# Kernel tuning notes

Measured on AMD Instinct MI355X. Metric: run time of the kernel, lower is better.

## Reference

```python
import jax, jax.numpy as jnp
import numpy as np

WS = 12
NUM_HEADS = 6
EPS = 1e-5


def _ln(x, w, b):
    mu = jnp.mean(x, axis=-1, keepdims=True)
    var = jnp.var(x, axis=-1, keepdims=True)
    return (x - mu) * jax.lax.rsqrt(var + EPS) * w + b


def _lin(x, w, b):
    return jnp.einsum('...i,oi->...o', x, w) + b


def _window_partition(x, ws):
    # x: [B, C, H, W] -> [B*Nh*Nw, ws*ws, C]
    B, C, H, W = x.shape
    x = x.reshape(B, C, H // ws, ws, W // ws, ws)
    x = jnp.transpose(x, (0, 2, 4, 3, 5, 1))
    return x.reshape(-1, ws * ws, C)


def _window_reverse(win, ws, B, C, H, W):
    Nh, Nw = H // ws, W // ws
    x = win.reshape(B, Nh, Nw, ws, ws, C)
    x = jnp.transpose(x, (0, 5, 1, 3, 2, 4))
    return x.reshape(B, C, H, W)


def setup_inputs() -> dict:
    key = jax.random.key(0)
    ks = jax.random.split(key, 12)
    B, C, H, W = 4, 192, 240, 240
    hid = 4 * C
    s = 0.02
    return {
        'opt': jax.random.normal(ks[0], (B, C, H, W), jnp.float32),
        'sar': jax.random.normal(ks[1], (B, C, H, W), jnp.float32),
        'ln_q_w': jnp.ones((C,), jnp.float32), 'ln_q_b': jnp.zeros((C,), jnp.float32),
        'ln_kv_w': jnp.ones((C,), jnp.float32), 'ln_kv_b': jnp.zeros((C,), jnp.float32),
        'wq': jax.random.normal(ks[2], (C, C), jnp.float32) * s, 'bq': jnp.zeros((C,), jnp.float32),
        'wk': jax.random.normal(ks[3], (C, C), jnp.float32) * s, 'bk': jnp.zeros((C,), jnp.float32),
        'wv': jax.random.normal(ks[4], (C, C), jnp.float32) * s, 'bv': jnp.zeros((C,), jnp.float32),
        'wp': jax.random.normal(ks[5], (C, C), jnp.float32) * s, 'bp': jnp.zeros((C,), jnp.float32),
        'gw1': jax.random.normal(ks[6], (C, C), jnp.float32) * s, 'gb1': jnp.zeros((C,), jnp.float32),
        'gw2': jax.random.normal(ks[7], (C, C), jnp.float32) * s, 'gb2': jnp.zeros((C,), jnp.float32),
        'gamma': jnp.float32(0.1),
        'ln_o_w': jnp.ones((C,), jnp.float32), 'ln_o_b': jnp.zeros((C,), jnp.float32),
        'w1': jax.random.normal(ks[8], (hid, C), jnp.float32) * s, 'b1': jnp.zeros((hid,), jnp.float32),
        'w2': jax.random.normal(ks[9], (C, hid), jnp.float32) * s, 'b2': jnp.zeros((C,), jnp.float32),
    }


def reference(opt, sar, ln_q_w, ln_q_b, ln_kv_w, ln_kv_b, wq, bq, wk, bk, wv, bv,
              wp, bp, gw1, gb1, gw2, gb2, gamma, ln_o_w, ln_o_b, w1, b1, w2, b2):
    B, C, H, W = opt.shape
    Hh = NUM_HEADS
    hd = C // Hh
    scale = hd ** -0.5

    opt_tok = _window_partition(opt, WS)   # [Bn, N, C]
    sar_tok = _window_partition(sar, WS)
    Bn, N, _ = opt_tok.shape

    opt_ln = _ln(opt_tok, ln_q_w, ln_q_b)
    sar_ln = _ln(sar_tok, ln_kv_w, ln_kv_b)

    q = _lin(opt_ln, wq, bq).reshape(Bn, N, Hh, hd)
    k = _lin(sar_ln, wk, bk).reshape(Bn, N, Hh, hd)
    v = _lin(sar_ln, wv, bv).reshape(Bn, N, Hh, hd)

    attn = jnp.einsum('bnhd,bmhd->bhnm', q, k) * scale
    attn = jax.nn.softmax(attn, axis=-1)
    out = jnp.einsum('bhnm,bmhd->bnhd', attn, v).reshape(Bn, N, C)
    fused = _lin(out, wp, bp)

    # sigmoid gate on mean-pooled sar tokens
    g = jax.nn.sigmoid(_lin(jax.nn.gelu(_lin(jnp.mean(sar_ln, axis=1), gw1, gb1), approximate=False), gw2, gb2))
    fused = opt_tok + gamma * (g[:, None, :] * fused)

    h = _ln(fused, ln_o_w, ln_o_b)
    h = _lin(jax.nn.gelu(_lin(h, w1, b1), approximate=False), w2, b2)
    fused = fused + h

    return _window_reverse(fused, WS, B, C, H, W)
```

## Files before the change

### kernel.cpp

```cpp
#include <hip/hip_runtime.h>
#include <hip/hip_bf16.h>

#define ROWS 230400
#define CDIM 192
#define NTOK 144
#define NWIN 1600
#define PLANE 57600
#define HDIM 768

typedef __attribute__((ext_vector_type(8))) short bf16x8;
typedef __attribute__((ext_vector_type(4))) float f32x4;

__device__ __forceinline__ ushort f2bf(float f) {
  union { float f; unsigned u; } v; v.f = f;
  unsigned r = v.u + 0x7FFFu + ((v.u >> 16) & 1u);
  return (ushort)(r >> 16);
}
__device__ __forceinline__ float bf2f(ushort h) {
  union { unsigned u; float f; } v; v.u = ((unsigned)h) << 16;
  return v.f;
}
__device__ __forceinline__ float gelu_f(float x) {
  return 0.5f * x * (1.f + erff(x * 0.7071067811865475f));
}

struct CvtJobs {
  const float* src[8];
  ushort* dst[8];
  int n[8];
};
__global__ __launch_bounds__(256) void cvt_kernel(CvtJobs jobs) {
  int stride = gridDim.x * blockDim.x;
  int t0 = blockIdx.x * blockDim.x + threadIdx.x;
  for (int j = 0; j < 8; ++j) {
    const float* s = jobs.src[j]; ushort* d = jobs.dst[j]; int n = jobs.n[j];
    for (int e = t0; e < n; e += stride) d[e] = f2bf(s[e]);
  }
}

__global__ __launch_bounds__(256) void lnpart_kernel(
    const float* __restrict__ opt, const float* __restrict__ sar,
    const float* __restrict__ lnqw, const float* __restrict__ lnqb,
    const float* __restrict__ lnkw, const float* __restrict__ lnkb,
    ushort* __restrict__ opt_ln, ushort* __restrict__ sar_ln,
    ushort* __restrict__ opt_tok) {
  __shared__ __align__(16) ushort X[NTOK * 200];
  __shared__ float smu[NTOK], srs[NTOK];
  int win = blockIdx.x;
  int b = win / 400, rr = win % 400, nh = rr / 20, nw = rr % 20;
  size_t wbase = (size_t)b * CDIM * PLANE + (size_t)(nh * 12) * 240 + nw * 12;
  int tid = threadIdx.x;
  for (int pass = 0; pass < 2; ++pass) {
    const float* src = pass ? sar : opt;
    for (int e = tid; e < CDIM * 36; e += 256) {
      int c = e / 36, r2 = e % 36, i = r2 / 3, j0 = (r2 % 3) * 4;
      float4 v = *(const float4*)&src[wbase + (size_t)c * PLANE + i * 240 + j0];
      int tok = i * 12 + j0;
      X[(tok + 0) * 200 + c] = f2bf(v.x);
      X[(tok + 1) * 200 + c] = f2bf(v.y);
      X[(tok + 2) * 200 + c] = f2bf(v.z);
      X[(tok + 3) * 200 + c] = f2bf(v.w);
    }
    __syncthreads();
    if (tid < NTOK) {
      float s = 0.f, qs = 0.f;
      for (int c = 0; c < CDIM; ++c) { float v = bf2f(X[tid * 200 + c]); s += v; qs += v * v; }
      float mu = s * (1.f / CDIM);
      smu[tid] = mu;
      srs[tid] = rsqrtf(qs * (1.f / CDIM) - mu * mu + 1e-5f);
    }
    __syncthreads();
    const float* w = pass ? lnkw : lnqw;
    const float* bb = pass ? lnkb : lnqb;
    ushort* dst = pass ? sar_ln : opt_ln;
    for (int e = tid; e < NTOK * CDIM; e += 256) {
      int tok = e / CDIM, c = e % CDIM;
      ushort raw = X[tok * 200 + c];
      float v = bf2f(raw);
      float y = (v - smu[tok]) * srs[tok] * w[c] + bb[c];
      size_t o = (size_t)(win * NTOK + tok) * CDIM + c;
      dst[o] = f2bf(y);
      if (!pass) opt_tok[o] = raw;
    }
    __syncthreads();
  }
}

enum { EPI_BF16 = 0, EPI_GELU = 1, EPI_SIG = 2, EPI_PROJ = 3 };

template <int EPI>
__global__ __launch_bounds__(256) void gemm_kernel(
    const ushort* __restrict__ A, const ushort* __restrict__ Wt,
    const float* __restrict__ bias, const float* __restrict__ bias2,
    void* __restrict__ outp, int M, int N, int K,
    const float* __restrict__ g, const ushort* __restrict__ opt_tok,
    const float* __restrict__ gamma_p) {
  __shared__ __align__(16) ushort Alds[128 * 40];
  int m0 = blockIdx.x * 128;
  int n0 = blockIdx.y * 64;
  int tid = threadIdx.x;
  int wave = tid >> 6, lane = tid & 63, ls = lane & 15, quad = lane >> 4;
  f32x4 acc[2][4] = {};
  for (int k0 = 0; k0 < K; k0 += 32) {
    for (int it = 0; it < 2; ++it) {
      int ch = tid + 256 * it;
      int r = ch >> 2, c8 = (ch & 3) * 8;
      int grow = m0 + r; if (grow > M - 1) grow = M - 1;
      *(bf16x8*)&Alds[r * 40 + c8] = *(const bf16x8*)&A[(size_t)grow * K + k0 + c8];
    }
    __syncthreads();
    int mb = wave * 32;
    bf16x8 af0 = *(const bf16x8*)&Alds[(mb + ls) * 40 + quad * 8];
    bf16x8 af1 = *(const bf16x8*)&Alds[(mb + 16 + ls) * 40 + quad * 8];
    bf16x8 bfr[4];
    for (int nf = 0; nf < 4; ++nf)
      bfr[nf] = *(const bf16x8*)&Wt[(size_t)(n0 + nf * 16 + ls) * K + k0 + quad * 8];
    for (int nf = 0; nf < 4; ++nf) {
      acc[0][nf] = __builtin_amdgcn_mfma_f32_16x16x32_bf16(af0, bfr[nf], acc[0][nf], 0, 0, 0);
      acc[1][nf] = __builtin_amdgcn_mfma_f32_16x16x32_bf16(af1, bfr[nf], acc[1][nf], 0, 0, 0);
    }
    __syncthreads();
  }
  float gam = (EPI == EPI_PROJ) ? gamma_p[0] : 0.f;
  for (int s = 0; s < 2; ++s) {
    int rowbase = m0 + wave * 32 + s * 16 + quad * 4;
    for (int nf = 0; nf < 4; ++nf) {
      int col = n0 + nf * 16 + ls;
      float bb = (col < 192) ? bias[col] : bias2[col - 192];
      for (int r = 0; r < 4; ++r) {
        int row = rowbase + r;
        if (row >= M) continue;
        float v = acc[s][nf][r] + bb;
        if (EPI == EPI_BF16) {
          ((ushort*)outp)[(size_t)row * N + col] = f2bf(v);
        } else if (EPI == EPI_GELU) {
          ((ushort*)outp)[(size_t)row * N + col] = f2bf(gelu_f(v));
        } else if (EPI == EPI_SIG) {
          ((float*)outp)[(size_t)row * N + col] = 1.f / (1.f + __expf(-v));
        } else {
          int win = row / NTOK;
          float gv = g[(size_t)win * CDIM + col];
          float ov = bf2f(opt_tok[(size_t)row * CDIM + col]);
          ((ushort*)outp)[(size_t)row * CDIM + col] = f2bf(ov + gam * gv * v);
        }
      }
    }
  }
}

__global__ __launch_bounds__(192) void pool_kernel(const ushort* __restrict__ sar_ln,
                                                   ushort* __restrict__ pool) {
  int win = blockIdx.x, c = threadIdx.x;
  float s = 0.f;
  size_t base = (size_t)win * NTOK * CDIM + c;
  for (int t = 0; t < NTOK; ++t) s += bf2f(sar_ln[base + (size_t)t * CDIM]);
  pool[(size_t)win * CDIM + c] = f2bf(s * (1.f / NTOK));
}

__global__ __launch_bounds__(256) void attn_kernel(const ushort* __restrict__ q,
                                                   const ushort* __restrict__ kv,
                                                   ushort* __restrict__ attn_out) {
  __shared__ __align__(16) ushort vT[32 * 168];
  __shared__ __align__(16) ushort P[4][16 * 168];
  int blk = blockIdx.x;
  int win = blk / 6, head = blk % 6;
  int tid = threadIdx.x, wave = tid >> 6, lane = tid & 63, ls = lane & 15, quad = lane >> 4;
  size_t qbase = (size_t)win * NTOK * CDIM + head * 32;
  size_t kbase = (size_t)win * NTOK * 384 + head * 32;
  size_t vbase = kbase + 192;
  for (int e = tid; e < NTOK * 32; e += 256) {
    int t = e >> 5, d = e & 31;
    vT[d * 168 + t] = kv[vbase + (size_t)t * 384 + d];
  }
  for (int e = tid; e < 32 * 24; e += 256) {
    int d = e / 24, j = 144 + e % 24;
    vT[d * 168 + j] = 0;
  }
  __syncthreads();
  const float scale = 0.17677669529663687f;
  ushort* Pw = P[wave];
  f32x4 zero = {0.f, 0.f, 0.f, 0.f};
  for (int mt = wave; mt < 9; mt += 4) {
    int m0 = mt * 16;
    bf16x8 aq = *(const bf16x8*)&q[qbase + (size_t)(m0 + ls) * CDIM + quad * 8];
    f32x4 S[9];
    for (int nt = 0; nt < 9; ++nt) {
      bf16x8 bk = *(const bf16x8*)&kv[kbase + (size_t)(nt * 16 + ls) * 384 + quad * 8];
      S[nt] = __builtin_amdgcn_mfma_f32_16x16x32_bf16(aq, bk, zero, 0, 0, 0);
    }
    for (int nt = 0; nt < 9; ++nt)
      for (int r = 0; r < 4; ++r) S[nt][r] *= scale;
    for (int r = 0; r < 4; ++r) {
      float mx = -1e30f;
      for (int nt = 0; nt < 9; ++nt) mx = fmaxf(mx, S[nt][r]);
      for (int o = 1; o < 16; o <<= 1) mx = fmaxf(mx, __shfl_xor(mx, o));
      float sm = 0.f;
      for (int nt = 0; nt < 9; ++nt) { float e = __expf(S[nt][r] - mx); S[nt][r] = e; sm += e; }
      for (int o = 1; o < 16; o <<= 1) sm += __shfl_xor(sm, o);
      float inv = 1.f / sm;
      for (int nt = 0; nt < 9; ++nt)
        Pw[(quad * 4 + r) * 168 + nt * 16 + ls] = f2bf(S[nt][r] * inv);
    }
    for (int e = lane; e < 16 * 24; e += 64) {
      int r = e / 24, j = 144 + e % 24;
      Pw[r * 168 + j] = 0;
    }
    f32x4 O[2] = {};
    for (int ks = 0; ks < 5; ++ks) {
      bf16x8 ap = *(const bf16x8*)&Pw[ls * 168 + ks * 32 + quad * 8];
      for (int dt = 0; dt < 2; ++dt) {
        bf16x8 bv = *(const bf16x8*)&vT[(dt * 16 + ls) * 168 + ks * 32 + quad * 8];
        O[dt] = __builtin_amdgcn_mfma_f32_16x16x32_bf16(ap, bv, O[dt], 0, 0, 0);
      }
    }
    for (int dt = 0; dt < 2; ++dt)
      for (int r = 0; r < 4; ++r)
        attn_out[(size_t)(win * NTOK + m0 + quad * 4 + r) * CDIM + head * 32 + dt * 16 + ls] =
            f2bf(O[dt][r]);
  }
}

__global__ __launch_bounds__(256) void lno_kernel(const ushort* __restrict__ x,
                                                  const float* __restrict__ w,
                                                  const float* __restrict__ b,
                                                  ushort* __restrict__ out) {
  int row = blockIdx.x * 4 + (threadIdx.x >> 6);
  int lane = threadIdx.x & 63;
  const ushort* xr = x + (size_t)row * CDIM;
  float v[3], s = 0.f, qs = 0.f;
  for (int i = 0; i < 3; ++i) { v[i] = bf2f(xr[lane + 64 * i]); s += v[i]; qs += v[i] * v[i]; }
  for (int o = 1; o < 64; o <<= 1) { s += __shfl_xor(s, o); qs += __shfl_xor(qs, o); }
  float mu = s * (1.f / CDIM);
  float rs = rsqrtf(qs * (1.f / CDIM) - mu * mu + 1e-5f);
  ushort* orow = out + (size_t)row * CDIM;
  for (int i = 0; i < 3; ++i) {
    int c = lane + 64 * i;
    orow[c] = f2bf((v[i] - mu) * rs * w[c] + b[c]);
  }
}

__global__ __launch_bounds__(256, 2) void mlp_kernel(
    const ushort* __restrict__ h, const ushort* __restrict__ fused,
    const ushort* __restrict__ w1b, const float* __restrict__ b1,
    const ushort* __restrict__ w2b, const float* __restrict__ b2,
    ushort* __restrict__ y) {
  __shared__ __align__(16) ushort Hs[128 * 200];
  __shared__ __align__(16) ushort Ts[128 * 72];
  int m0 = blockIdx.x * 128;
  int tid = threadIdx.x, wave = tid >> 6, lane = tid & 63, ls = lane & 15, quad = lane >> 4;
  for (int it = 0; it < 12; ++it) {
    int ch = tid + 256 * it;
    int r = ch / 24, c8 = (ch % 24) * 8;
    *(bf16x8*)&Hs[r * 200 + c8] = *(const bf16x8*)&h[(size_t)(m0 + r) * CDIM + c8];
  }
  __syncthreads();
  int mb = wave * 32;
  f32x4 acc[2][12] = {};
  for (int hc = 0; hc < HDIM; hc += 64) {
    f32x4 t[2][4] = {};
    for (int ks = 0; ks < 6; ++ks) {
      bf16x8 a0 = *(const bf16x8*)&Hs[(mb + ls) * 200 + ks * 32 + quad * 8];
      bf16x8 a1 = *(const bf16x8*)&Hs[(mb + 16 + ls) * 200 + ks * 32 + quad * 8];
      for (int nf = 0; nf < 4; ++nf) {
        bf16x8 bw = *(const bf16x8*)&w1b[(size_t)(hc + nf * 16 + ls) * CDIM + ks * 32 + quad * 8];
        t[0][nf] = __builtin_amdgcn_mfma_f32_16x16x32_bf16(a0, bw, t[0][nf], 0, 0, 0);
        t[1][nf] = __builtin_amdgcn_mfma_f32_16x16x32_bf16(a1, bw, t[1][nf], 0, 0, 0);
      }
    }
    for (int s = 0; s < 2; ++s)
      for (int nf = 0; nf < 4; ++nf) {
        float bb = b1[hc + nf * 16 + ls];
        for (int r = 0; r < 4; ++r) {
          float v = gelu_f(t[s][nf][r] + bb);
          Ts[(mb + s * 16 + quad * 4 + r) * 72 + nf * 16 + ls] = f2bf(v);
        }
      }
    for (int ks = 0; ks < 2; ++ks) {
      bf16x8 a0 = *(const bf16x8*)&Ts[(mb + ls) * 72 + ks * 32 + quad * 8];
      bf16x8 a1 = *(const bf16x8*)&Ts[(mb + 16 + ls) * 72 + ks * 32 + quad * 8];
      for (int nf = 0; nf < 12; ++nf) {
        bf16x8 bw = *(const bf16x8*)&w2b[(size_t)(nf * 16 + ls) * HDIM + hc + ks * 32 + quad * 8];
        acc[0][nf] = __builtin_amdgcn_mfma_f32_16x16x32_bf16(a0, bw, acc[0][nf], 0, 0, 0);
        acc[1][nf] = __builtin_amdgcn_mfma_f32_16x16x32_bf16(a1, bw, acc[1][nf], 0, 0, 0);
      }
    }
  }
  for (int s = 0; s < 2; ++s)
    for (int nf = 0; nf < 12; ++nf) {
      float bb = b2[nf * 16 + ls];
      for (int r = 0; r < 4; ++r) {
        size_t idx = (size_t)(m0 + mb + s * 16 + quad * 4 + r) * CDIM + nf * 16 + ls;
        y[idx] = f2bf(bf2f(fused[idx]) + acc[s][nf][r] + bb);
      }
    }
}

__global__ __launch_bounds__(256) void unpart_kernel(const ushort* __restrict__ y,
                                                     float* __restrict__ out) {
  __shared__ __align__(16) ushort X[NTOK * 200];
  int win = blockIdx.x;
  int b = win / 400, rr = win % 400, nh = rr / 20, nw = rr % 20;
  size_t wbase = (size_t)b * CDIM * PLANE + (size_t)(nh * 12) * 240 + nw * 12;
  int tid = threadIdx.x;
  for (int e = tid; e < NTOK * 24; e += 256) {
    int tok = e / 24, c8 = (e % 24) * 8;
    *(bf16x8*)&X[tok * 200 + c8] = *(const bf16x8*)&y[(size_t)(win * NTOK + tok) * CDIM + c8];
  }
  __syncthreads();
  for (int e = tid; e < CDIM * 36; e += 256) {
    int c = e / 36, r2 = e % 36, i = r2 / 3, j0 = (r2 % 3) * 4;
    int tok = i * 12 + j0;
    float4 v;
    v.x = bf2f(X[(tok + 0) * 200 + c]);
    v.y = bf2f(X[(tok + 1) * 200 + c]);
    v.z = bf2f(X[(tok + 2) * 200 + c]);
    v.w = bf2f(X[(tok + 3) * 200 + c]);
    *(float4*)&out[wbase + (size_t)c * PLANE + i * 240 + j0] = v;
  }
}

extern "C" void kernel_launch(void* const* d_in, const int* in_sizes, int n_in,
                              void* d_out, int out_size, void* d_ws, size_t ws_size,
                              hipStream_t stream) {
  const float* opt   = (const float*)d_in[0];
  const float* sar   = (const float*)d_in[1];
  const float* lnqw  = (const float*)d_in[2];
  const float* lnqb  = (const float*)d_in[3];
  const float* lnkw  = (const float*)d_in[4];
  const float* lnkb  = (const float*)d_in[5];
  const float* wq    = (const float*)d_in[6];
  const float* bq    = (const float*)d_in[7];
  const float* wk    = (const float*)d_in[8];
  const float* bk    = (const float*)d_in[9];
  const float* wv    = (const float*)d_in[10];
  const float* bv    = (const float*)d_in[11];
  const float* wp    = (const float*)d_in[12];
  const float* bp    = (const float*)d_in[13];
  const float* gw1   = (const float*)d_in[14];
  const float* gb1   = (const float*)d_in[15];
  const float* gw2   = (const float*)d_in[16];
  const float* gb2   = (const float*)d_in[17];
  const float* gamma = (const float*)d_in[18];
  const float* lnow  = (const float*)d_in[19];
  const float* lnob  = (const float*)d_in[20];
  const float* w1    = (const float*)d_in[21];
  const float* b1    = (const float*)d_in[22];
  const float* w2    = (const float*)d_in[23];
  const float* b2    = (const float*)d_in[24];

  char* ws = (char*)d_ws;
  size_t off = 0;
  auto take = [&](size_t bytes) -> char* {
    char* p = ws + off;
    off += (bytes + 255) & ~(size_t)255;
    return p;
  };
  const size_t big = (size_t)ROWS * CDIM * 2;
  ushort* opt_ln  = (ushort*)take(big);
  ushort* sar_ln  = (ushort*)take(big);
  ushort* opt_tok = (ushort*)take(big);
  ushort* qb      = (ushort*)take(big);
  ushort* kv      = (ushort*)take((size_t)ROWS * 384 * 2);
  ushort* wq_bf   = (ushort*)take(CDIM * CDIM * 2);
  ushort* wkv_bf  = (ushort*)take(2 * CDIM * CDIM * 2);
  ushort* wp_bf   = (ushort*)take(CDIM * CDIM * 2);
  ushort* w1_bf   = (ushort*)take((size_t)HDIM * CDIM * 2);
  ushort* w2_bf   = (ushort*)take((size_t)CDIM * HDIM * 2);
  ushort* gw1_bf  = (ushort*)take(CDIM * CDIM * 2);
  ushort* gw2_bf  = (ushort*)take(CDIM * CDIM * 2);
  ushort* pool_bf = (ushort*)take(NWIN * CDIM * 2);
  ushort* g1_bf   = (ushort*)take(NWIN * CDIM * 2);
  float*  g_f     = (float*)take(NWIN * CDIM * 4);
  ushort* h        = opt_ln;
  ushort* attn_out = sar_ln;
  ushort* fused    = qb;
  ushort* yb       = sar_ln;

  CvtJobs jobs;
  jobs.src[0] = wq;  jobs.dst[0] = wq_bf;               jobs.n[0] = CDIM * CDIM;
  jobs.src[1] = wk;  jobs.dst[1] = wkv_bf;              jobs.n[1] = CDIM * CDIM;
  jobs.src[2] = wv;  jobs.dst[2] = wkv_bf + CDIM * CDIM; jobs.n[2] = CDIM * CDIM;
  jobs.src[3] = wp;  jobs.dst[3] = wp_bf;               jobs.n[3] = CDIM * CDIM;
  jobs.src[4] = w1;  jobs.dst[4] = w1_bf;               jobs.n[4] = HDIM * CDIM;
  jobs.src[5] = w2;  jobs.dst[5] = w2_bf;               jobs.n[5] = CDIM * HDIM;
  jobs.src[6] = gw1; jobs.dst[6] = gw1_bf;              jobs.n[6] = CDIM * CDIM;
  jobs.src[7] = gw2; jobs.dst[7] = gw2_bf;              jobs.n[7] = CDIM * CDIM;
  cvt_kernel<<<dim3(128), dim3(256), 0, stream>>>(jobs);

  lnpart_kernel<<<dim3(NWIN), dim3(256), 0, stream>>>(
      opt, sar, lnqw, lnqb, lnkw, lnkb, opt_ln, sar_ln, opt_tok);

  gemm_kernel<EPI_BF16><<<dim3(1800, 3), dim3(256), 0, stream>>>(
      opt_ln, wq_bf, bq, bq, (void*)qb, ROWS, CDIM, CDIM, nullptr, nullptr, nullptr);
  gemm_kernel<EPI_BF16><<<dim3(1800, 6), dim3(256), 0, stream>>>(
      sar_ln, wkv_bf, bk, bv, (void*)kv, ROWS, 384, CDIM, nullptr, nullptr, nullptr);

  pool_kernel<<<dim3(NWIN), dim3(192), 0, stream>>>(sar_ln, pool_bf);
  gemm_kernel<EPI_GELU><<<dim3(13, 3), dim3(256), 0, stream>>>(
      pool_bf, gw1_bf, gb1, gb1, (void*)g1_bf, NWIN, CDIM, CDIM, nullptr, nullptr, nullptr);
  gemm_kernel<EPI_SIG><<<dim3(13, 3), dim3(256), 0, stream>>>(
      g1_bf, gw2_bf, gb2, gb2, (void*)g_f, NWIN, CDIM, CDIM, nullptr, nullptr, nullptr);

  attn_kernel<<<dim3(NWIN * 6), dim3(256), 0, stream>>>(qb, kv, attn_out);

  gemm_kernel<EPI_PROJ><<<dim3(1800, 3), dim3(256), 0, stream>>>(
      attn_out, wp_bf, bp, bp, (void*)fused, ROWS, CDIM, CDIM, g_f, opt_tok, gamma);

  lno_kernel<<<dim3(ROWS / 4), dim3(256), 0, stream>>>(fused, lnow, lnob, h);

  mlp_kernel<<<dim3(1800), dim3(256), 0, stream>>>(h, fused, w1_bf, b1, w2_bf, b2, yb);

  unpart_kernel<<<dim3(NWIN), dim3(256), 0, stream>>>(yb, (float*)d_out);
}
```

Before: 2.269 ms.

## Fuse QKV GEMMs, fuse projection with output LayerNorm, retile MLP, use tanh GELU

Q, K and V projections now run in one launch that keeps the whole K dimension in LDS. The output projection absorbs the gated residual and the output LayerNorm, which removes the separate LN kernel and one round trip of the fused tensor. The MLP kernel moves to 64-row tiles with per-wave scratch so each CU can hold more blocks. Smaller edits switch GELU from exact erf to the tanh approximation, pad the LDS row stride in lnpart, and hoist attention's P padding zero-fill out of the loop. The tanh GELU changes numerics slightly, and the larger LDS tiles may limit occupancy.

```diff
diff --git a/kernel.cpp b/kernel.cpp
--- a/kernel.cpp
+++ b/kernel.cpp
@@ -21,7 +21,10 @@
   return v.f;
 }
 __device__ __forceinline__ float gelu_f(float x) {
-  return 0.5f * x * (1.f + erff(x * 0.7071067811865475f));
+  float u = 1.5957691216057308f * (x + 0.044715f * x * x * x);
+  float e = __expf(u);
+  float t = 1.f - 2.f / (e + 1.f);
+  return 0.5f * x * (1.f + t);
 }
 
 struct CvtJobs {
@@ -38,13 +41,14 @@
   }
 }
 
+#define XSTR 194
 __global__ __launch_bounds__(256) void lnpart_kernel(
     const float* __restrict__ opt, const float* __restrict__ sar,
     const float* __restrict__ lnqw, const float* __restrict__ lnqb,
     const float* __restrict__ lnkw, const float* __restrict__ lnkb,
     ushort* __restrict__ opt_ln, ushort* __restrict__ sar_ln,
     ushort* __restrict__ opt_tok) {
-  __shared__ __align__(16) ushort X[NTOK * 200];
+  __shared__ __align__(16) ushort X[NTOK * XSTR];
   __shared__ float smu[NTOK], srs[NTOK];
   int win = blockIdx.x;
   int b = win / 400, rr = win % 400, nh = rr / 20, nw = rr % 20;
@@ -56,15 +60,20 @@
       int c = e / 36, r2 = e % 36, i = r2 / 3, j0 = (r2 % 3) * 4;
       float4 v = *(const float4*)&src[wbase + (size_t)c * PLANE + i * 240 + j0];
       int tok = i * 12 + j0;
-      X[(tok + 0) * 200 + c] = f2bf(v.x);
-      X[(tok + 1) * 200 + c] = f2bf(v.y);
-      X[(tok + 2) * 200 + c] = f2bf(v.z);
-      X[(tok + 3) * 200 + c] = f2bf(v.w);
+      X[(tok + 0) * XSTR + c] = f2bf(v.x);
+      X[(tok + 1) * XSTR + c] = f2bf(v.y);
+      X[(tok + 2) * XSTR + c] = f2bf(v.z);
+      X[(tok + 3) * XSTR + c] = f2bf(v.w);
     }
     __syncthreads();
     if (tid < NTOK) {
+      const uint* row = (const uint*)&X[tid * XSTR];
       float s = 0.f, qs = 0.f;
-      for (int c = 0; c < CDIM; ++c) { float v = bf2f(X[tid * 200 + c]); s += v; qs += v * v; }
+      for (int i = 0; i < 96; ++i) {
+        uint u = row[i];
+        float a = bf2f((ushort)(u & 0xffffu)), bb2 = bf2f((ushort)(u >> 16));
+        s += a + bb2; qs += a * a + bb2 * bb2;
+      }
       float mu = s * (1.f / CDIM);
       smu[tid] = mu;
       srs[tid] = rsqrtf(qs * (1.f / CDIM) - mu * mu + 1e-5f);
@@ -75,7 +84,7 @@
     ushort* dst = pass ? sar_ln : opt_ln;
     for (int e = tid; e < NTOK * CDIM; e += 256) {
       int tok = e / CDIM, c = e % CDIM;
-      ushort raw = X[tok * 200 + c];
+      ushort raw = X[tok * XSTR + c];
       float v = bf2f(raw);
       float y = (v - smu[tok]) * srs[tok] * w[c] + bb[c];
       size_t o = (size_t)(win * NTOK + tok) * CDIM + c;
@@ -86,15 +95,52 @@
   }
 }
 
-enum { EPI_BF16 = 0, EPI_GELU = 1, EPI_SIG = 2, EPI_PROJ = 3 };
-
+__global__ __launch_bounds__(256, 3) void qkv_kernel(
+    const ushort* __restrict__ opt_ln, const ushort* __restrict__ sar_ln,
+    const ushort* __restrict__ wq_bf, const ushort* __restrict__ wkv_bf,
+    const float* __restrict__ bq, const float* __restrict__ bk,
+    const float* __restrict__ bv,
+    ushort* __restrict__ qb, ushort* __restrict__ kvb) {
+  __shared__ __align__(16) ushort Alds[128 * 200];
+  int y = blockIdx.y;
+  const ushort* A; const ushort* Wt; ushort* out; int N, n0;
+  if (y < 3) { A = opt_ln; Wt = wq_bf;  out = qb;  N = 192; n0 = y * 64; }
+  else       { A = sar_ln; Wt = wkv_bf; out = kvb; N = 384; n0 = (y - 3) * 64; }
+  int m0 = blockIdx.x * 128;
+  int tid = threadIdx.x, wave = tid >> 6, lane = tid & 63, ls = lane & 15, quad = lane >> 4;
+  for (int it = 0; it < 12; ++it) {
+    int ch = tid + 256 * it;
+    int r = ch / 24, c8 = (ch % 24) * 8;
+    *(bf16x8*)&Alds[r * 200 + c8] = *(const bf16x8*)&A[(size_t)(m0 + r) * CDIM + c8];
+  }
+  __syncthreads();
+  int mb = wave * 32;
+  f32x4 acc[2][4] = {};
+  for (int k0 = 0; k0 < CDIM; k0 += 32) {
+    bf16x8 af0 = *(const bf16x8*)&Alds[(mb + ls) * 200 + k0 + quad * 8];
+    bf16x8 af1 = *(const bf16x8*)&Alds[(mb + 16 + ls) * 200 + k0 + quad * 8];
+    for (int nf = 0; nf < 4; ++nf) {
+      bf16x8 bw = *(const bf16x8*)&Wt[(size_t)(n0 + nf * 16 + ls) * CDIM + k0 + quad * 8];
+      acc[0][nf] = __builtin_amdgcn_mfma_f32_16x16x32_bf16(af0, bw, acc[0][nf], 0, 0, 0);
+      acc[1][nf] = __builtin_amdgcn_mfma_f32_16x16x32_bf16(af1, bw, acc[1][nf], 0, 0, 0);
+    }
+  }
+  for (int s = 0; s < 2; ++s) {
+    int rowbase = m0 + mb + s * 16 + quad * 4;
+    for (int nf = 0; nf < 4; ++nf) {
+      int col = n0 + nf * 16 + ls;
+      float bb = (y < 3) ? bq[col] : ((col < 192) ? bk[col] : bv[col - 192]);
+      for (int r = 0; r < 4; ++r)
+        out[(size_t)(rowbase + r) * N + col] = f2bf(acc[s][nf][r] + bb);
+    }
+  }
+}
+
+enum { EPI_GELU = 1, EPI_SIG = 2 };
 template <int EPI>
 __global__ __launch_bounds__(256) void gemm_kernel(
     const ushort* __restrict__ A, const ushort* __restrict__ Wt,
-    const float* __restrict__ bias, const float* __restrict__ bias2,
-    void* __restrict__ outp, int M, int N, int K,
-    const float* __restrict__ g, const ushort* __restrict__ opt_tok,
-    const float* __restrict__ gamma_p) {
+    const float* __restrict__ bias, void* __restrict__ outp, int M, int N, int K) {
   __shared__ __align__(16) ushort Alds[128 * 40];
   int m0 = blockIdx.x * 128;
   int n0 = blockIdx.y * 64;
@@ -112,37 +158,24 @@
     int mb = wave * 32;
     bf16x8 af0 = *(const bf16x8*)&Alds[(mb + ls) * 40 + quad * 8];
     bf16x8 af1 = *(const bf16x8*)&Alds[(mb + 16 + ls) * 40 + quad * 8];
-    bf16x8 bfr[4];
-    for (int nf = 0; nf < 4; ++nf)
-      bfr[nf] = *(const bf16x8*)&Wt[(size_t)(n0 + nf * 16 + ls) * K + k0 + quad * 8];
     for (int nf = 0; nf < 4; ++nf) {
-      acc[0][nf] = __builtin_amdgcn_mfma_f32_16x16x32_bf16(af0, bfr[nf], acc[0][nf], 0, 0, 0);
-      acc[1][nf] = __builtin_amdgcn_mfma_f32_16x16x32_bf16(af1, bfr[nf], acc[1][nf], 0, 0, 0);
+      bf16x8 bw = *(const bf16x8*)&Wt[(size_t)(n0 + nf * 16 + ls) * K + k0 + quad * 8];
+      acc[0][nf] = __builtin_amdgcn_mfma_f32_16x16x32_bf16(af0, bw, acc[0][nf], 0, 0, 0);
+      acc[1][nf] = __builtin_amdgcn_mfma_f32_16x16x32_bf16(af1, bw, acc[1][nf], 0, 0, 0);
     }
     __syncthreads();
   }
-  float gam = (EPI == EPI_PROJ) ? gamma_p[0] : 0.f;
   for (int s = 0; s < 2; ++s) {
     int rowbase = m0 + wave * 32 + s * 16 + quad * 4;
     for (int nf = 0; nf < 4; ++nf) {
       int col = n0 + nf * 16 + ls;
-      float bb = (col < 192) ? bias[col] : bias2[col - 192];
+      float bb = bias[col];
       for (int r = 0; r < 4; ++r) {
         int row = rowbase + r;
         if (row >= M) continue;
         float v = acc[s][nf][r] + bb;
-        if (EPI == EPI_BF16) {
-          ((ushort*)outp)[(size_t)row * N + col] = f2bf(v);
-        } else if (EPI == EPI_GELU) {
-          ((ushort*)outp)[(size_t)row * N + col] = f2bf(gelu_f(v));
-        } else if (EPI == EPI_SIG) {
-          ((float*)outp)[(size_t)row * N + col] = 1.f / (1.f + __expf(-v));
-        } else {
-          int win = row / NTOK;
-          float gv = g[(size_t)win * CDIM + col];
-          float ov = bf2f(opt_tok[(size_t)row * CDIM + col]);
-          ((ushort*)outp)[(size_t)row * CDIM + col] = f2bf(ov + gam * gv * v);
-        }
+        if (EPI == EPI_GELU) ((ushort*)outp)[(size_t)row * N + col] = f2bf(gelu_f(v));
+        else ((float*)outp)[(size_t)row * N + col] = 1.f / (1.f + __expf(-v));
       }
     }
   }
@@ -176,9 +209,13 @@
     int d = e / 24, j = 144 + e % 24;
     vT[d * 168 + j] = 0;
   }
+  ushort* Pw = P[wave];
+  for (int e = lane; e < 16 * 24; e += 64) {
+    int r = e / 24, j = 144 + e % 24;
+    Pw[r * 168 + j] = 0;
+  }
   __syncthreads();
   const float scale = 0.17677669529663687f;
-  ushort* Pw = P[wave];
   f32x4 zero = {0.f, 0.f, 0.f, 0.f};
   for (int mt = wave; mt < 9; mt += 4) {
     int m0 = mt * 16;
@@ -201,10 +238,6 @@
       for (int nt = 0; nt < 9; ++nt)
         Pw[(quad * 4 + r) * 168 + nt * 16 + ls] = f2bf(S[nt][r] * inv);
     }
-    for (int e = lane; e < 16 * 24; e += 64) {
-      int r = e / 24, j = 144 + e % 24;
-      Pw[r * 168 + j] = 0;
-    }
     f32x4 O[2] = {};
     for (int ks = 0; ks < 5; ++ks) {
       bf16x8 ap = *(const bf16x8*)&Pw[ls * 168 + ks * 32 + quad * 8];
@@ -220,79 +253,105 @@
   }
 }
 
-__global__ __launch_bounds__(256) void lno_kernel(const ushort* __restrict__ x,
-                                                  const float* __restrict__ w,
-                                                  const float* __restrict__ b,
-                                                  ushort* __restrict__ out) {
-  int row = blockIdx.x * 4 + (threadIdx.x >> 6);
-  int lane = threadIdx.x & 63;
-  const ushort* xr = x + (size_t)row * CDIM;
-  float v[3], s = 0.f, qs = 0.f;
-  for (int i = 0; i < 3; ++i) { v[i] = bf2f(xr[lane + 64 * i]); s += v[i]; qs += v[i] * v[i]; }
-  for (int o = 1; o < 64; o <<= 1) { s += __shfl_xor(s, o); qs += __shfl_xor(qs, o); }
-  float mu = s * (1.f / CDIM);
-  float rs = rsqrtf(qs * (1.f / CDIM) - mu * mu + 1e-5f);
-  ushort* orow = out + (size_t)row * CDIM;
-  for (int i = 0; i < 3; ++i) {
-    int c = lane + 64 * i;
-    orow[c] = f2bf((v[i] - mu) * rs * w[c] + b[c]);
-  }
-}
-
-__global__ __launch_bounds__(256, 2) void mlp_kernel(
-    const ushort* __restrict__ h, const ushort* __restrict__ fused,
-    const ushort* __restrict__ w1b, const float* __restrict__ b1,
-    const ushort* __restrict__ w2b, const float* __restrict__ b2,
-    ushort* __restrict__ y) {
-  __shared__ __align__(16) ushort Hs[128 * 200];
-  __shared__ __align__(16) ushort Ts[128 * 72];
+__global__ __launch_bounds__(256, 2) void projln_kernel(
+    const ushort* __restrict__ A, const ushort* __restrict__ wp_bf,
+    const float* __restrict__ bp, const float* __restrict__ g,
+    const ushort* __restrict__ opt_tok, const float* __restrict__ gamma_p,
+    const float* __restrict__ lnow, const float* __restrict__ lnob,
+    ushort* __restrict__ fused, ushort* __restrict__ h) {
+  __shared__ __align__(16) ushort Alds[128 * 200];
   int m0 = blockIdx.x * 128;
   int tid = threadIdx.x, wave = tid >> 6, lane = tid & 63, ls = lane & 15, quad = lane >> 4;
   for (int it = 0; it < 12; ++it) {
     int ch = tid + 256 * it;
     int r = ch / 24, c8 = (ch % 24) * 8;
-    *(bf16x8*)&Hs[r * 200 + c8] = *(const bf16x8*)&h[(size_t)(m0 + r) * CDIM + c8];
+    *(bf16x8*)&Alds[r * 200 + c8] = *(const bf16x8*)&A[(size_t)(m0 + r) * CDIM + c8];
   }
   __syncthreads();
   int mb = wave * 32;
   f32x4 acc[2][12] = {};
+  for (int k0 = 0; k0 < CDIM; k0 += 32) {
+    bf16x8 af0 = *(const bf16x8*)&Alds[(mb + ls) * 200 + k0 + quad * 8];
+    bf16x8 af1 = *(const bf16x8*)&Alds[(mb + 16 + ls) * 200 + k0 + quad * 8];
+    for (int nf = 0; nf < 12; ++nf) {
+      bf16x8 bw = *(const bf16x8*)&wp_bf[(size_t)(nf * 16 + ls) * CDIM + k0 + quad * 8];
+      acc[0][nf] = __builtin_amdgcn_mfma_f32_16x16x32_bf16(af0, bw, acc[0][nf], 0, 0, 0);
+      acc[1][nf] = __builtin_amdgcn_mfma_f32_16x16x32_bf16(af1, bw, acc[1][nf], 0, 0, 0);
+    }
+  }
+  float gam = gamma_p[0];
+  for (int s = 0; s < 2; ++s) {
+    for (int r = 0; r < 4; ++r) {
+      int rg = m0 + mb + s * 16 + quad * 4 + r;
+      int win = rg / NTOK;
+      float fv[12], s1 = 0.f, s2 = 0.f;
+      for (int nf = 0; nf < 12; ++nf) {
+        int col = nf * 16 + ls;
+        float v = acc[s][nf][r] + bp[col];
+        float f = bf2f(opt_tok[(size_t)rg * CDIM + col]) + gam * g[(size_t)win * CDIM + col] * v;
+        fv[nf] = f; s1 += f; s2 += f * f;
+      }
+      for (int o = 1; o < 16; o <<= 1) { s1 += __shfl_xor(s1, o); s2 += __shfl_xor(s2, o); }
+      float mu = s1 * (1.f / CDIM);
+      float rs = rsqrtf(s2 * (1.f / CDIM) - mu * mu + 1e-5f);
+      for (int nf = 0; nf < 12; ++nf) {
+        int col = nf * 16 + ls;
+        size_t idx = (size_t)rg * CDIM + col;
+        fused[idx] = f2bf(fv[nf]);
+        h[idx] = f2bf((fv[nf] - mu) * rs * lnow[col] + lnob[col]);
+      }
+    }
+  }
+}
+
+__global__ __launch_bounds__(256, 3) void mlp_kernel(
+    const ushort* __restrict__ h, const ushort* __restrict__ fused,
+    const ushort* __restrict__ w1b, const float* __restrict__ b1,
+    const ushort* __restrict__ w2b, const float* __restrict__ b2,
+    ushort* __restrict__ y) {
+  __shared__ __align__(16) ushort Hs[64 * 200];
+  __shared__ __align__(16) ushort Ts[4][16 * 72];
+  int m0 = blockIdx.x * 64;
+  int tid = threadIdx.x, wave = tid >> 6, lane = tid & 63, ls = lane & 15, quad = lane >> 4;
+  for (int it = 0; it < 6; ++it) {
+    int ch = tid + 256 * it;
+    int r = ch / 24, c8 = (ch % 24) * 8;
+    *(bf16x8*)&Hs[r * 200 + c8] = *(const bf16x8*)&h[(size_t)(m0 + r) * CDIM + c8];
+  }
+  __syncthreads();
+  int mb = wave * 16;
+  ushort* Tw = Ts[wave];
+  f32x4 acc[12] = {};
+#pragma unroll 1
   for (int hc = 0; hc < HDIM; hc += 64) {
-    f32x4 t[2][4] = {};
+    f32x4 t[4] = {};
     for (int ks = 0; ks < 6; ++ks) {
-      bf16x8 a0 = *(const bf16x8*)&Hs[(mb + ls) * 200 + ks * 32 + quad * 8];
-      bf16x8 a1 = *(const bf16x8*)&Hs[(mb + 16 + ls) * 200 + ks * 32 + quad * 8];
+      bf16x8 a = *(const bf16x8*)&Hs[(mb + ls) * 200 + ks * 32 + quad * 8];
       for (int nf = 0; nf < 4; ++nf) {
         bf16x8 bw = *(const bf16x8*)&w1b[(size_t)(hc + nf * 16 + ls) * CDIM + ks * 32 + quad * 8];
-        t[0][nf] = __builtin_amdgcn_mfma_f32_16x16x32_bf16(a0, bw, t[0][nf], 0, 0, 0);
-        t[1][nf] = __builtin_amdgcn_mfma_f32_16x16x32_bf16(a1, bw, t[1][nf], 0, 0, 0);
-      }
-    }
-    for (int s = 0; s < 2; ++s)
-      for (int nf = 0; nf < 4; ++nf) {
-        float bb = b1[hc + nf * 16 + ls];
-        for (int r = 0; r < 4; ++r) {
-          float v = gelu_f(t[s][nf][r] + bb);
-          Ts[(mb + s * 16 + quad * 4 + r) * 72 + nf * 16 + ls] = f2bf(v);
-        }
-      }
+        t[nf] = __builtin_amdgcn_mfma_f32_16x16x32_bf16(a, bw, t[nf], 0, 0, 0);
+      }
+    }
+    for (int nf = 0; nf < 4; ++nf) {
+      float bb = b1[hc + nf * 16 + ls];
+      for (int r = 0; r < 4; ++r)
+        Tw[(quad * 4 + r) * 72 + nf * 16 + ls] = f2bf(gelu_f(t[nf][r] + bb));
+    }
     for (int ks = 0; ks < 2; ++ks) {
-      bf16x8 a0 = *(const bf16x8*)&Ts[(mb + ls) * 72 + ks * 32 + quad * 8];
-      bf16x8 a1 = *(const bf16x8*)&Ts[(mb + 16 + ls) * 72 + ks * 32 + quad * 8];
+      bf16x8 ap = *(const bf16x8*)&Tw[ls * 72 + ks * 32 + quad * 8];
       for (int nf = 0; nf < 12; ++nf) {
         bf16x8 bw = *(const bf16x8*)&w2b[(size_t)(nf * 16 + ls) * HDIM + hc + ks * 32 + quad * 8];
-        acc[0][nf] = __builtin_amdgcn_mfma_f32_16x16x32_bf16(a0, bw, acc[0][nf], 0, 0, 0);
-        acc[1][nf] = __builtin_amdgcn_mfma_f32_16x16x32_bf16(a1, bw, acc[1][nf], 0, 0, 0);
-      }
-    }
-  }
-  for (int s = 0; s < 2; ++s)
-    for (int nf = 0; nf < 12; ++nf) {
-      float bb = b2[nf * 16 + ls];
-      for (int r = 0; r < 4; ++r) {
-        size_t idx = (size_t)(m0 + mb + s * 16 + quad * 4 + r) * CDIM + nf * 16 + ls;
-        y[idx] = f2bf(bf2f(fused[idx]) + acc[s][nf][r] + bb);
-      }
-    }
+        acc[nf] = __builtin_amdgcn_mfma_f32_16x16x32_bf16(ap, bw, acc[nf], 0, 0, 0);
+      }
+    }
+  }
+  for (int nf = 0; nf < 12; ++nf) {
+    float bb = b2[nf * 16 + ls];
+    for (int r = 0; r < 4; ++r) {
+      size_t idx = (size_t)(m0 + mb + quad * 4 + r) * CDIM + nf * 16 + ls;
+      y[idx] = f2bf(bf2f(fused[idx]) + acc[nf][r] + bb);
+    }
+  }
 }
 
 __global__ __launch_bounds__(256) void unpart_kernel(const ushort* __restrict__ y,
@@ -390,25 +449,21 @@
   lnpart_kernel<<<dim3(NWIN), dim3(256), 0, stream>>>(
       opt, sar, lnqw, lnqb, lnkw, lnkb, opt_ln, sar_ln, opt_tok);
 
-  gemm_kernel<EPI_BF16><<<dim3(1800, 3), dim3(256), 0, stream>>>(
-      opt_ln, wq_bf, bq, bq, (void*)qb, ROWS, CDIM, CDIM, nullptr, nullptr, nullptr);
-  gemm_kernel<EPI_BF16><<<dim3(1800, 6), dim3(256), 0, stream>>>(
-      sar_ln, wkv_bf, bk, bv, (void*)kv, ROWS, 384, CDIM, nullptr, nullptr, nullptr);
+  qkv_kernel<<<dim3(1800, 9), dim3(256), 0, stream>>>(
+      opt_ln, sar_ln, wq_bf, wkv_bf, bq, bk, bv, qb, kv);
 
   pool_kernel<<<dim3(NWIN), dim3(192), 0, stream>>>(sar_ln, pool_bf);
   gemm_kernel<EPI_GELU><<<dim3(13, 3), dim3(256), 0, stream>>>(
-      pool_bf, gw1_bf, gb1, gb1, (void*)g1_bf, NWIN, CDIM, CDIM, nullptr, nullptr, nullptr);
+      pool_bf, gw1_bf, gb1, (void*)g1_bf, NWIN, CDIM, CDIM);
   gemm_kernel<EPI_SIG><<<dim3(13, 3), dim3(256), 0, stream>>>(
-      g1_bf, gw2_bf, gb2, gb2, (void*)g_f, NWIN, CDIM, CDIM, nullptr, nullptr, nullptr);
+      g1_bf, gw2_bf, gb2, (void*)g_f, NWIN, CDIM, CDIM);
 
   attn_kernel<<<dim3(NWIN * 6), dim3(256), 0, stream>>>(qb, kv, attn_out);
 
-  gemm_kernel<EPI_PROJ><<<dim3(1800, 3), dim3(256), 0, stream>>>(
-      attn_out, wp_bf, bp, bp, (void*)fused, ROWS, CDIM, CDIM, g_f, opt_tok, gamma);
-
-  lno_kernel<<<dim3(ROWS / 4), dim3(256), 0, stream>>>(fused, lnow, lnob, h);
-
-  mlp_kernel<<<dim3(1800), dim3(256), 0, stream>>>(h, fused, w1_bf, b1, w2_bf, b2, yb);
+  projln_kernel<<<dim3(1800), dim3(256), 0, stream>>>(
+      attn_out, wp_bf, bp, g_f, opt_tok, gamma, lnow, lnob, fused, h);
+
+  mlp_kernel<<<dim3(3600), dim3(256), 0, stream>>>(h, fused, w1_bf, b1, w2_bf, b2, yb);
 
   unpart_kernel<<<dim3(NWIN), dim3(256), 0, stream>>>(yb, (float*)d_out);
 }
```

Measured after the change: 2.541 ms. 12.0% more time.
